# Kernel optimization log

Hardware: AMD Instinct MI355X
Metric: run time of the kernel (lower is better)

The kernel has to match this reference:

```python
import jax, jax.numpy as jnp
import numpy as np

B, T, C, H = 2, 2048, 1024, 16
D = C // H  # head dim = 64

def setup_inputs() -> dict:
    key = jax.random.key(0)
    k1, k2 = jax.random.split(key)
    x = jax.random.normal(k1, (B, T, C), dtype=jnp.float32)
    W_attn = jax.random.normal(k2, (3 * C, C), dtype=jnp.float32) * 0.02
    return {"x": x, "W_attn": W_attn}

def reference(x, W_attn):
    Bx, Tx, Cx = x.shape
    qkv = jnp.einsum('btc,fc->btf', x, W_attn)  # fused QKV projection (bias=False)
    q, k, v = jnp.split(qkv, 3, axis=-1)
    # [B, H, T, D]
    q = q.reshape(Bx, Tx, H, D).transpose(0, 2, 1, 3)
    k = k.reshape(Bx, Tx, H, D).transpose(0, 2, 1, 3)
    v = v.reshape(Bx, Tx, H, D).transpose(0, 2, 1, 3)
    scale = 1.0 / jnp.sqrt(jnp.asarray(D, dtype=q.dtype))
    scores = jnp.einsum('bhqd,bhkd->bhqk', q, k) * scale  # [B,H,T,T]
    causal = jnp.tril(jnp.ones((Tx, Tx), dtype=bool))
    scores = jnp.where(causal[None, None], scores, jnp.asarray(-jnp.inf, dtype=scores.dtype))
    attn = jax.nn.softmax(scores, axis=-1)
    y = jnp.einsum('bhqk,bhkd->bhqd', attn, v)
    y = y.transpose(0, 2, 1, 3).reshape(Bx, Tx, Cx)  # merge heads; dropout=0 at eval
    return y
```

## Files before the change

kernel.cpp:

```cpp
#include <hip/hip_runtime.h>
#include <hip/hip_bf16.h>

#define Bn 2
#define Tn 2048
#define Cn 1024
#define Hn 16
#define Dn 64
#define Mdim 4096
#define Ndim 3072
#define Kdim 1024

typedef unsigned short u16;
typedef __attribute__((ext_vector_type(8))) short bf16x8;
typedef __attribute__((ext_vector_type(4))) float f32x4;

__device__ __forceinline__ u16 f2bf(float v) {
    unsigned int x = __builtin_bit_cast(unsigned int, v);
    unsigned int r = (x + 0x7fffu + ((x >> 16) & 1u)) >> 16;
    return (u16)r;
}

__device__ __forceinline__ unsigned int pack2(float a, float b) {
    return (unsigned int)f2bf(a) | ((unsigned int)f2bf(b) << 16);
}

__device__ __forceinline__ unsigned int cvt_pk_bf16(float lo, float hi) {
    unsigned int r;
    asm("v_cvt_pk_bf16_f32 %0, %1, %2" : "=v"(r) : "v"(lo), "v"(hi));
    return r;
}

__device__ __forceinline__ void async16(const void* g, void* l) {
    __builtin_amdgcn_global_load_lds(
        (const __attribute__((address_space(1))) void*)g,
        (__attribute__((address_space(3))) void*)(unsigned int)(unsigned long long)l,
        16, 0, 0);
}

__device__ __forceinline__ int probe_inline(const unsigned int* __restrict__ X, int tid) {
    const int lane = tid & 63;
    int cnt = 0;
    #pragma unroll
    for (int i = 0; i < 8; i++) {
        unsigned int e = (X[lane * 8 + i] >> 7) & 0xFFu;
        cnt += (e >= 100u && e < 134u) ? 1 : 0;
    }
    #pragma unroll
    for (int off = 1; off < 64; off <<= 1) cnt += __shfl_xor(cnt, off);
    return cnt > 256 ? 1 : 0;
}

#define NXC ((size_t)Mdim * Kdim / 8)
#define NWC ((size_t)Ndim * Kdim / 8)

__global__ __launch_bounds__(256) void convert_in(
        const void* __restrict__ Xv, const void* __restrict__ Wv,
        u16* __restrict__ Xb, u16* __restrict__ Wb, int* __restrict__ flag) {
    const int isbf = probe_inline((const unsigned int*)Xv, threadIdx.x);
    if (blockIdx.x == 0 && threadIdx.x == 0) *flag = isbf;
    size_t i = (size_t)blockIdx.x * 256 + threadIdx.x;
    if (i >= NXC + NWC) return;
    const void* src; u16* dst; size_t off;
    if (i < NXC) { src = Xv; dst = Xb; off = i; }
    else         { src = Wv; dst = Wb; off = i - NXC; }
    if (isbf) {
        ((uint4*)dst)[off] = ((const uint4*)src)[off];
    } else {
        const float4* s = (const float4*)src + off * 2;
        float4 a = s[0], b = s[1];
        ((uint4*)dst)[off] = (uint4){pack2(a.x, a.y), pack2(a.z, a.w),
                                     pack2(b.x, b.y), pack2(b.z, b.w)};
    }
}

#define NTq (Kdim / 64)

#define PBAR() do { asm volatile("" ::: "memory"); \
                    __builtin_amdgcn_s_barrier();  \
                    asm volatile("" ::: "memory"); } while (0)
#define VMW(n) asm volatile("s_waitcnt vmcnt(" #n ")" ::: "memory")

#define STGA(QIDX, BUF, KOFF) \
    async16(Xb + (size_t)(m0 + (QIDX) * 64 + srow) * Kdim + (KOFF) + gc, \
            &sA[BUF][(QIDX) * 4096 + w * 512])
#define STGB(QIDX, BUF, KOFF) \
    async16(Wb + (size_t)(n0 + (QIDX) * 64 + srow) * Kdim + (KOFF) + gc, \
            &sB[BUF][(QIDX) * 4096 + w * 512])

#define RDAh(FR, MQ, BUF) do {                                             \
    _Pragma("unroll")                                                      \
    for (int mt = 0; mt < 4; mt++) {                                       \
        const u16* p = &sA[BUF][(wm + (MQ) * 64 + mt * 16 + r16) * 64];    \
        FR[mt][0] = *(const bf16x8*)(p + cx0);                             \
        FR[mt][1] = *(const bf16x8*)(p + (cx0 ^ 32));                      \
    } } while (0)

#define RDBall(BUF) do {                                                   \
    _Pragma("unroll")                                                      \
    for (int nt = 0; nt < 3; nt++) {                                       \
        const u16* p = &sB[BUF][(wn + nt * 16 + r16) * 64];                \
        bfr[nt][0] = *(const bf16x8*)(p + cx0);                            \
        bfr[nt][1] = *(const bf16x8*)(p + (cx0 ^ 32));                     \
    } } while (0)

#define MMH(BASE, FR) do {                                                 \
    _Pragma("unroll")                                                      \
    for (int mt = 0; mt < 4; mt++)                                         \
        _Pragma("unroll")                                                  \
        for (int nt = 0; nt < 3; nt++) {                                   \
            acc[(BASE)+mt][nt] = __builtin_amdgcn_mfma_f32_16x16x32_bf16(  \
                FR[mt][0], bfr[nt][0], acc[(BASE)+mt][nt], 0, 0, 0);       \
            acc[(BASE)+mt][nt] = __builtin_amdgcn_mfma_f32_16x16x32_bf16(  \
                FR[mt][1], bfr[nt][1], acc[(BASE)+mt][nt], 0, 0, 0);       \
        }                                                                  \
} while (0)

__global__ __launch_bounds__(512, 2) void qkv_gemm(
        const u16* __restrict__ Xb, const u16* __restrict__ Wb,
        u16* __restrict__ Q, u16* __restrict__ Kc, u16* __restrict__ Vt) {
    __shared__ __align__(16) u16 sA[2][256 * 64];
    __shared__ __align__(16) u16 sB[2][192 * 64];

    const int tid  = threadIdx.x;
    const int lane = tid & 63;
    const int w    = tid >> 6;
    const int quad = lane >> 4;
    const int r16  = lane & 15;
    const int wm   = (w >> 2) * 128;
    const int wn   = (w & 3) * 48;

    const int l0 = blockIdx.x;
    const int nl = (l0 & 7) * 32 + (l0 >> 3);
    const int m0 = (nl >> 4) * 256;
    const int n0 = (nl & 15) * 192;

    const int lr   = lane >> 3;
    const int gc   = ((lane & 7) ^ lr) * 8;
    const int srow = w * 8 + lr;

    const int cx0 = (quad ^ (r16 & 7)) * 8;

    f32x4 acc[8][3];
    #pragma unroll
    for (int i = 0; i < 8; i++)
        #pragma unroll
        for (int j = 0; j < 3; j++)
            acc[i][j] = (f32x4){0.f, 0.f, 0.f, 0.f};

    bf16x8 af[4][2], ag[4][2];
    bf16x8 bfr[3][2];

    #pragma unroll
    for (int q = 0; q < 4; q++) STGA(q, 0, 0);
    #pragma unroll
    for (int q = 0; q < 3; q++) STGB(q, 0, 0);
    VMW(0);
    PBAR();

    int koff = 0;
    for (int kt = 0; kt < NTq; kt++) {
        const int cur = kt & 1, nxt = cur ^ 1;
        const int kn = koff + 64;
        if (kt + 1 < NTq) {
            #pragma unroll
            for (int q = 0; q < 4; q++) STGA(q, nxt, kn);
            #pragma unroll
            for (int q = 0; q < 3; q++) STGB(q, nxt, kn);
            VMW(7);
        } else {
            VMW(0);
        }
        PBAR();
        RDAh(af, 0, cur);
        RDBall(cur);
        RDAh(ag, 1, cur);
        __builtin_amdgcn_s_setprio(1);
        MMH(0, af);
        MMH(4, ag);
        __builtin_amdgcn_s_setprio(0);
        PBAR();
        koff = kn;
    }

    #pragma unroll
    for (int mh = 0; mh < 2; mh++)
    #pragma unroll
    for (int mt = 0; mt < 4; mt++)
    #pragma unroll
    for (int nt = 0; nt < 3; nt++) {
        f32x4 v4 = acc[mh * 4 + mt][nt];
        const int mBase = m0 + wm + mh * 64 + mt * 16 + quad * 4;
        const int f = n0 + wn + nt * 16 + r16;
        const int sect = f >> 10;
        const int b = mBase >> 11;
        const int t0 = mBase & 2047;
        const int h = (f >> 6) & 15;
        const int d = f & 63;
        const int bh = b * Hn + h;
        if (sect == 0) {
            #pragma unroll
            for (int r = 0; r < 4; r++)
                Q[((size_t)(bh * Tn + t0 + r)) * Dn + d] = f2bf(v4[r] * 0.125f);
        } else if (sect == 1) {
            #pragma unroll
            for (int r = 0; r < 4; r++)
                Kc[((size_t)(bh * Tn + t0 + r)) * Dn + d] = f2bf(v4[r]);
        } else {
            ushort4 pk4 = {f2bf(v4[0]), f2bf(v4[1]), f2bf(v4[2]), f2bf(v4[3])};
            *(ushort4*)(Vt + ((size_t)(bh * Dn + d)) * Tn + t0) = pk4;
        }
    }
}


#define SWZ(R, C) ((R) * 64 + (((C) * 8) ^ (((R) & 7) << 3)))

#define ASTG(KB, BUF) do {                                                     \
    const int kbase_ = (KB) * 64;                                              \
    if (w < 2) {                                                               \
        _Pragma("unroll")                                                      \
        for (int i_ = 0; i_ < 4; i_++) {                                       \
            const int seg = w * 4 + i_;            \
            async16(Kc + qkBase + (size_t)(kbase_ + seg * 8 + rl) * Dn + gc8,  \
                    &sK[BUF][seg * 512]);                                      \
        }                                                                      \
    } else {                                                                   \
        _Pragma("unroll")                                                      \
        for (int i_ = 0; i_ < 4; i_++) {                                       \
            const int seg = (w - 2) * 4 + i_;    \
            async16(Vt + vBase + (size_t)(seg * 8 + rl) * Tn + kbase_ + gc8,   \
                    &sV[BUF][seg * 512]);                                      \
        }                                                                      \
    }                                                                          \
} while (0)

#define ACOMP(KB, BUF) do {                                                    \
    const int kbase_ = (KB) * 64;                                              \
    const bool diag_ = ((KB) == nkb - 1);                                      \
    bf16x8 kf[4][2], vf[4][2];                                                 \
    _Pragma("unroll")                                                          \
    for (int nt = 0; nt < 4; nt++) {                                           \
        kf[nt][0] = *(const bf16x8*)&sK[BUF][SWZ(nt * 16 + r16, quad)];        \
        kf[nt][1] = *(const bf16x8*)&sK[BUF][SWZ(nt * 16 + r16, 4 + quad)];    \
    }                                                                          \
    _Pragma("unroll")                                                          \
    for (int dt = 0; dt < 4; dt++) {                                           \
        vf[dt][0] = *(const bf16x8*)&sV[BUF][SWZ(dt * 16 + r16, quad)];        \
        vf[dt][1] = *(const bf16x8*)&sV[BUF][SWZ(dt * 16 + r16, 4 + quad)];    \
    }                                                                          \
    _Pragma("unroll")                                                          \
    for (int mt = 0; mt < 2; mt++) {                                           \
        f32x4 s[4];                                                            \
        __builtin_amdgcn_s_setprio(1);                                         \
        _Pragma("unroll")                                                      \
        for (int nt = 0; nt < 4; nt++) {                                       \
            f32x4 z = (f32x4){-8.f, -8.f, -8.f, -8.f};                         \
            z = __builtin_amdgcn_mfma_f32_16x16x32_bf16(kf[nt][0], aq[mt][0], z, 0, 0, 0); \
            z = __builtin_amdgcn_mfma_f32_16x16x32_bf16(kf[nt][1], aq[mt][1], z, 0, 0, 0); \
            s[nt] = z;                                                         \
        }                                                                      \
        __builtin_amdgcn_s_setprio(0);                                         \
        if (diag_) {                                                           \
            const int query = qw0 + mt * 16 + r16;                             \
            _Pragma("unroll")                                                  \
            for (int nt = 0; nt < 4; nt++)                                     \
                _Pragma("unroll")                                              \
                for (int r = 0; r < 4; r++) {                                  \
                    int key = kbase_ + nt * 16 + quad * 4 + r;                 \
                    if (key > query) s[nt][r] = -1e30f;                        \
                }                                                              \
        }                                                                      \
        unsigned int pk[4][2];                                                 \
        _Pragma("unroll")                                                      \
        for (int nt = 0; nt < 4; nt++) {                                       \
            float p0 = __expf(s[nt][0]);                                       \
            float p1 = __expf(s[nt][1]);                                       \
            float p2 = __expf(s[nt][2]);                                       \
            float p3 = __expf(s[nt][3]);                                       \
            lacc[mt] += (p0 + p1) + (p2 + p3);                                 \
            pk[nt][0] = cvt_pk_bf16(p0, p1);                                   \
            pk[nt][1] = cvt_pk_bf16(p2, p3);                                   \
        }                                                                      \
        _Pragma("unroll")                                                      \
        for (int kc = 0; kc < 2; kc++) {                                       \
            int4 bq;                                                           \
            _Pragma("unroll")                                                  \
            for (int h_ = 0; h_ < 2; h_++) {                                   \
                unsigned int a = pk[kc * 2 + 0][h_];                           \
                unsigned int b = pk[kc * 2 + 1][h_];                           \
                auto t = __builtin_amdgcn_permlane32_swap(a, b, false, false); \
                auto u = __builtin_amdgcn_permlane16_swap(t[0], t[1], false, false); \
                ((unsigned int*)&bq)[0 + h_] = u[0];                           \
                ((unsigned int*)&bq)[2 + h_] = u[1];                           \
            }                                                                  \
            bf16x8 bqv = __builtin_bit_cast(bf16x8, bq);                       \
            __builtin_amdgcn_s_setprio(1);                                     \
            _Pragma("unroll")                                                  \
            for (int dt = 0; dt < 4; dt++)                                     \
                o[mt][dt] = __builtin_amdgcn_mfma_f32_16x16x32_bf16(           \
                    vf[dt][kc], bqv, o[mt][dt], 0, 0, 0);                      \
            __builtin_amdgcn_s_setprio(0);                                     \
        }                                                                      \
    }                                                                          \
} while (0)

__global__ __launch_bounds__(256, 2) void attn(
        const u16* __restrict__ Q, const u16* __restrict__ Kc,
        const u16* __restrict__ Vt, void* __restrict__ Y,
        const int* __restrict__ flag) {
    __shared__ __align__(16) u16 sK[4][4096];
    __shared__ __align__(16) u16 sV[4][4096];

    const int isbf = *flag;
    const int tid  = threadIdx.x;
    const int lane = tid & 63;
    const int w    = tid >> 6;
    const int quad = lane >> 4;
    const int r16  = lane & 15;
    const int bid  = blockIdx.x;
    const int bh   = bid & (Bn * Hn - 1);
    const int half = bid >> 8;
    const int j    = (bid & 255) >> 5;
    const int qt   = half ? j : (15 - j);
    const int qw0  = qt * 128 + w * 32;
    const int nt   = 2 * qt + 2;
    const int nkb  = 2 * qt + 1 + (w >> 1);
    const size_t qkBase = (size_t)bh * Tn * Dn;
    const size_t vBase  = (size_t)bh * Dn * Tn;
    const int bb = bh >> 4, hh = bh & 15;

    const int rl  = lane >> 3;
    const int gc8 = (((lane & 7) ^ rl)) * 8;

    bf16x8 aq[2][2];
    #pragma unroll
    for (int mt = 0; mt < 2; mt++) {
        const u16* qp = Q + qkBase + (size_t)(qw0 + mt * 16 + r16) * Dn;
        aq[mt][0] = *(const bf16x8*)(qp + quad * 8);
        aq[mt][1] = *(const bf16x8*)(qp + 32 + quad * 8);
    }

    float lacc[2] = {0.f, 0.f};
    f32x4 o[2][4];
    #pragma unroll
    for (int mt = 0; mt < 2; mt++)
        #pragma unroll
        for (int dt = 0; dt < 4; dt++) o[mt][dt] = (f32x4){0.f, 0.f, 0.f, 0.f};

    ASTG(0, 0);
    ASTG(1, 1);
    VMW(4);
    PBAR();

    for (int i = 0; i < nt; i++) {
        if (i + 2 < nt)      { ASTG(i + 2, (i + 2) & 3); VMW(8); }
        else if (i + 1 < nt) { VMW(4); }
        else                 { VMW(0); }
        PBAR();
        if (i < nkb) ACOMP(i, i & 3);
    }

    #pragma unroll
    for (int mt = 0; mt < 2; mt++) {
        float den = lacc[mt];
        den += __shfl_xor(den, 16);
        den += __shfl_xor(den, 32);
        float rden = 1.f / fmaxf(den, 1e-30f);
        int t = qw0 + mt * 16 + r16;
        #pragma unroll
        for (int dt = 0; dt < 4; dt++) {
            float v0 = o[mt][dt][0] * rden;
            float v1 = o[mt][dt][1] * rden;
            float v2 = o[mt][dt][2] * rden;
            float v3 = o[mt][dt][3] * rden;
            int c = hh * Dn + dt * 16 + quad * 4;
            size_t idx = ((size_t)(bb * Tn + t)) * Cn + c;
            if (isbf) {
                ushort4 pk4 = {f2bf(v0), f2bf(v1), f2bf(v2), f2bf(v3)};
                *(ushort4*)((u16*)Y + idx) = pk4;
            } else {
                float4 f4 = {v0, v1, v2, v3};
                *(float4*)((float*)Y + idx) = f4;
            }
        }
    }
}

extern "C" void kernel_launch(void* const* d_in, const int* in_sizes, int n_in,
                              void* d_out, int out_size, void* d_ws, size_t ws_size,
                              hipStream_t stream) {
    const void* X = d_in[0];
    const void* W = d_in[1];
    void* Y = d_out;

    const size_t per = (size_t)Bn * Hn * Tn * Dn;
    int* flag = (int*)d_ws;
    u16* Q  = (u16*)((char*)d_ws + 256);
    u16* Kc = Q + per;
    u16* Vt = Kc + per;
    u16* Xb = Vt + per;
    u16* Wb = Xb + (size_t)Mdim * Kdim;

    {
        const size_t nch = NXC + NWC;
        convert_in<<<dim3((unsigned)((nch + 255) / 256)), 256, 0, stream>>>(X, W, Xb, Wb, flag);
    }
    qkv_gemm<<<dim3((Mdim / 256) * (Ndim / 192)), 512, 0, stream>>>(Xb, Wb, Q, Kc, Vt);
    attn<<<dim3(Bn * Hn * (Tn / 128)), 256, 0, stream>>>(Q, Kc, Vt, Y, flag);
}
```

Before: 142.4 us.

## Split GEMM k-loop into half-tile stages and use exp2 softmax with packed conversions

```diff
diff --git a/kernel.cpp b/kernel.cpp
--- a/kernel.cpp
+++ b/kernel.cpp
@@ -18,10 +18,6 @@
     unsigned int x = __builtin_bit_cast(unsigned int, v);
     unsigned int r = (x + 0x7fffu + ((x >> 16) & 1u)) >> 16;
     return (u16)r;
-}
-
-__device__ __forceinline__ unsigned int pack2(float a, float b) {
-    return (unsigned int)f2bf(a) | ((unsigned int)f2bf(b) << 16);
 }
 
 __device__ __forceinline__ unsigned int cvt_pk_bf16(float lo, float hi) {
@@ -68,12 +64,13 @@
     } else {
         const float4* s = (const float4*)src + off * 2;
         float4 a = s[0], b = s[1];
-        ((uint4*)dst)[off] = (uint4){pack2(a.x, a.y), pack2(a.z, a.w),
-                                     pack2(b.x, b.y), pack2(b.z, b.w)};
+        ((uint4*)dst)[off] = (uint4){cvt_pk_bf16(a.x, a.y), cvt_pk_bf16(a.z, a.w),
+                                     cvt_pk_bf16(b.x, b.y), cvt_pk_bf16(b.z, b.w)};
     }
 }
 
 #define NTq (Kdim / 64)
+#define QSCL 0.1803368867f
 
 #define PBAR() do { asm volatile("" ::: "memory"); \
                     __builtin_amdgcn_s_barrier();  \
@@ -154,28 +151,29 @@
     for (int q = 0; q < 4; q++) STGA(q, 0, 0);
     #pragma unroll
     for (int q = 0; q < 3; q++) STGB(q, 0, 0);
-    VMW(0);
+    STGA(0, 1, 64); STGA(2, 1, 64); STGB(0, 1, 64); STGB(1, 1, 64);
+    VMW(4);
     PBAR();
 
     int koff = 0;
     for (int kt = 0; kt < NTq; kt++) {
         const int cur = kt & 1, nxt = cur ^ 1;
-        const int kn = koff + 64;
-        if (kt + 1 < NTq) {
-            #pragma unroll
-            for (int q = 0; q < 4; q++) STGA(q, nxt, kn);
-            #pragma unroll
-            for (int q = 0; q < 3; q++) STGB(q, nxt, kn);
-            VMW(7);
-        } else {
-            VMW(0);
-        }
-        PBAR();
+        const int kn = koff + 64, kn2 = koff + 128;
+        if (kt + 1 < NTq) { STGA(1, nxt, kn); STGA(3, nxt, kn); STGB(2, nxt, kn); }
         RDAh(af, 0, cur);
         RDBall(cur);
-        RDAh(ag, 1, cur);
+        PBAR();
         __builtin_amdgcn_s_setprio(1);
         MMH(0, af);
+        __builtin_amdgcn_s_setprio(0);
+        PBAR();
+        RDAh(ag, 1, cur);
+        if (kt + 2 < NTq) { STGA(0, cur, kn2); STGA(2, cur, kn2);
+                            STGB(0, cur, kn2); STGB(1, cur, kn2); }
+        if (kt + 2 < NTq)      { VMW(4); }
+        else if (kt + 1 < NTq) { VMW(0); }
+        PBAR();
+        __builtin_amdgcn_s_setprio(1);
         MMH(4, ag);
         __builtin_amdgcn_s_setprio(0);
         PBAR();
@@ -198,16 +196,24 @@
         const int d = f & 63;
         const int bh = b * Hn + h;
         if (sect == 0) {
-            #pragma unroll
-            for (int r = 0; r < 4; r++)
-                Q[((size_t)(bh * Tn + t0 + r)) * Dn + d] = f2bf(v4[r] * 0.125f);
+            unsigned int u01 = cvt_pk_bf16(v4[0] * QSCL, v4[1] * QSCL);
+            unsigned int u23 = cvt_pk_bf16(v4[2] * QSCL, v4[3] * QSCL);
+            u16* qp = Q + ((size_t)(bh * Tn + t0)) * Dn + d;
+            qp[0]      = (u16)u01;
+            qp[Dn]     = (u16)(u01 >> 16);
+            qp[2 * Dn] = (u16)u23;
+            qp[3 * Dn] = (u16)(u23 >> 16);
         } else if (sect == 1) {
-            #pragma unroll
-            for (int r = 0; r < 4; r++)
-                Kc[((size_t)(bh * Tn + t0 + r)) * Dn + d] = f2bf(v4[r]);
+            unsigned int u01 = cvt_pk_bf16(v4[0], v4[1]);
+            unsigned int u23 = cvt_pk_bf16(v4[2], v4[3]);
+            u16* kp = Kc + ((size_t)(bh * Tn + t0)) * Dn + d;
+            kp[0]      = (u16)u01;
+            kp[Dn]     = (u16)(u01 >> 16);
+            kp[2 * Dn] = (u16)u23;
+            kp[3 * Dn] = (u16)(u23 >> 16);
         } else {
-            ushort4 pk4 = {f2bf(v4[0]), f2bf(v4[1]), f2bf(v4[2]), f2bf(v4[3])};
-            *(ushort4*)(Vt + ((size_t)(bh * Dn + d)) * Tn + t0) = pk4;
+            uint2 pk2 = {cvt_pk_bf16(v4[0], v4[1]), cvt_pk_bf16(v4[2], v4[3])};
+            *(uint2*)(Vt + ((size_t)(bh * Dn + d)) * Tn + t0) = pk2;
         }
     }
 }
@@ -254,7 +260,7 @@
         __builtin_amdgcn_s_setprio(1);                                         \
         _Pragma("unroll")                                                      \
         for (int nt = 0; nt < 4; nt++) {                                       \
-            f32x4 z = (f32x4){-8.f, -8.f, -8.f, -8.f};                         \
+            f32x4 z = (f32x4){-11.5415603f, -11.5415603f, -11.5415603f, -11.5415603f}; \
             z = __builtin_amdgcn_mfma_f32_16x16x32_bf16(kf[nt][0], aq[mt][0], z, 0, 0, 0); \
             z = __builtin_amdgcn_mfma_f32_16x16x32_bf16(kf[nt][1], aq[mt][1], z, 0, 0, 0); \
             s[nt] = z;                                                         \
@@ -273,10 +279,10 @@
         unsigned int pk[4][2];                                                 \
         _Pragma("unroll")                                                      \
         for (int nt = 0; nt < 4; nt++) {                                       \
-            float p0 = __expf(s[nt][0]);                                       \
-            float p1 = __expf(s[nt][1]);                                       \
-            float p2 = __expf(s[nt][2]);                                       \
-            float p3 = __expf(s[nt][3]);                                       \
+            float p0 = __builtin_amdgcn_exp2f(s[nt][0]);                       \
+            float p1 = __builtin_amdgcn_exp2f(s[nt][1]);                       \
+            float p2 = __builtin_amdgcn_exp2f(s[nt][2]);                       \
+            float p3 = __builtin_amdgcn_exp2f(s[nt][3]);                       \
             lacc[mt] += (p0 + p1) + (p2 + p3);                                 \
             pk[nt][0] = cvt_pk_bf16(p0, p1);                                   \
             pk[nt][1] = cvt_pk_bf16(p2, p3);                                   \
@@ -376,8 +382,8 @@
             int c = hh * Dn + dt * 16 + quad * 4;
             size_t idx = ((size_t)(bb * Tn + t)) * Cn + c;
             if (isbf) {
-                ushort4 pk4 = {f2bf(v0), f2bf(v1), f2bf(v2), f2bf(v3)};
-                *(ushort4*)((u16*)Y + idx) = pk4;
+                uint2 pk2 = {cvt_pk_bf16(v0, v1), cvt_pk_bf16(v2, v3)};
+                *(uint2*)((u16*)Y + idx) = pk2;
             } else {
                 float4 f4 = {v0, v1, v2, v3};
                 *(float4*)((float*)Y + idx) = f4;
```

After: 140.1 us. About the same (-1.7%).
